# Optimization experiments

Hardware: AMD Instinct MI355X
Metric: run time of the kernel (lower is better)

Reference implementation:

```python
import jax, jax.numpy as jnp
import numpy as np

EMBED_DIM = 1024
NUM_HEADS = 16
HEAD_DIM = EMBED_DIM // NUM_HEADS


def setup_inputs() -> dict:
    key = jax.random.key(0)
    ks = jax.random.split(key, 10)
    B, S, E = 2, 2048, EMBED_DIM
    scale = 1.0 / np.sqrt(E)
    x = jax.random.normal(ks[0], (B, S, E), dtype=jnp.float32)
    mask = jax.random.randint(ks[1], (B, 1, S, S), 0, 2, dtype=jnp.int32)
    # Linear weights stored as [in, out] (transposed torch layout for x @ W)
    Wq = jax.random.normal(ks[2], (E, E), dtype=jnp.float32) * scale
    bq = jnp.zeros((E,), dtype=jnp.float32)
    Wk = jax.random.normal(ks[3], (E, E), dtype=jnp.float32) * scale
    bk = jnp.zeros((E,), dtype=jnp.float32)
    Wv = jax.random.normal(ks[4], (E, E), dtype=jnp.float32) * scale
    bv = jnp.zeros((E,), dtype=jnp.float32)
    Wo = jax.random.normal(ks[5], (E, E), dtype=jnp.float32) * scale
    bo = jnp.zeros((E,), dtype=jnp.float32)
    return {"x": x, "mask": mask, "Wq": Wq, "bq": bq, "Wk": Wk, "bk": bk,
            "Wv": Wv, "bv": bv, "Wo": Wo, "bo": bo}


def _heads(t, B, S):
    # [B, S, E] -> [B, H, S, Dh]
    return t.reshape(B, S, NUM_HEADS, HEAD_DIM).transpose(0, 2, 1, 3)


def reference(x, mask, Wq, bq, Wk, bk, Wv, bv, Wo, bo):
    B, S, E = x.shape
    q = _heads(x @ Wq + bq, B, S)
    k = _heads(x @ Wk + bk, B, S)
    v = _heads(x @ Wv + bv, B, S)
    inv_sqrt_dk = 1.0 / jnp.sqrt(jnp.asarray(HEAD_DIM, dtype=x.dtype))
    # scores: [B, H, S, S]
    scores = jnp.einsum('bhqd,bhkd->bhqk', q, k) * inv_sqrt_dk
    scores = jnp.where(mask == 0, jnp.asarray(-1e9, dtype=scores.dtype), scores)
    p = jax.nn.softmax(scores, axis=-1)
    ctx = jnp.einsum('bhqk,bhkd->bhqd', p, v)  # [B, H, S, Dh]
    ctx = ctx.transpose(0, 2, 1, 3).reshape(B, S, E)
    return ctx @ Wo + bo
```

## Files before the change

### kernel.cpp

```cpp
#include <hip/hip_runtime.h>

typedef float f32x4 __attribute__((ext_vector_type(4)));
typedef short s16x8 __attribute__((ext_vector_type(8)));
typedef unsigned short u16;
typedef unsigned short u16x4 __attribute__((ext_vector_type(4)));
typedef unsigned int u32x2 __attribute__((ext_vector_type(2)));

#define DI __device__ __forceinline__

constexpr int B_ = 2, S_ = 2048, E_ = 1024, H_ = 16, DH = 64, M_ = B_ * S_;
constexpr float QSCALE = 0.125f * 1.4426950408889634f;

DI u16 f2bf(float f) {
    unsigned u = __float_as_uint(f);
    u += 0x7fffu + ((u >> 16) & 1u);
    return (u16)(u >> 16);
}

DI unsigned cvtpk(float lo, float hi) {
    unsigned r;
    asm("v_cvt_pk_bf16_f32 %0, %1, %2" : "=v"(r) : "v"(lo), "v"(hi));
    return r;
}

DI void mfma(f32x4& d, s16x8 a, s16x8 b) {
    asm("v_mfma_f32_16x16x32_bf16 %0, %1, %2, %0" : "+v"(d) : "v"(a), "v"(b));
}

typedef __attribute__((address_space(1))) const void gas_cv;
typedef __attribute__((address_space(3))) void las_v;
DI void gl16(const void* g, void* l) {
    __builtin_amdgcn_global_load_lds((gas_cv*)g, (las_v*)l, 16, 0, 0);
}


__global__ __launch_bounds__(256) void cvt_bf16(const float* __restrict__ in,
                                                u16* __restrict__ out, int n4) {
    int i = blockIdx.x * 256 + threadIdx.x;
    if (i < n4) {
        float4 v = ((const float4*)in)[i];
        u16x4 o;
        o.x = f2bf(v.x); o.y = f2bf(v.y); o.z = f2bf(v.z); o.w = f2bf(v.w);
        ((u16x4*)out)[i] = o;
    }
}

__global__ __launch_bounds__(256) void wtrans(const float* __restrict__ in,
                                              u16* __restrict__ out) {
    __shared__ float t[64][65];
    int k0 = blockIdx.x * 64, n0 = blockIdx.y * 64;
    int tx = threadIdx.x & 63, ty = threadIdx.x >> 6;
#pragma unroll
    for (int i = 0; i < 16; i++) {
        int r = i * 4 + ty;
        t[r][tx] = in[(k0 + r) * E_ + n0 + tx];
    }
    __syncthreads();
#pragma unroll
    for (int i = 0; i < 16; i++) {
        int r = i * 4 + ty;
        out[(n0 + r) * E_ + k0 + tx] = f2bf(t[tx][r]);
    }
}

__global__ __launch_bounds__(256) void mpackK(const int* __restrict__ mask,
                                              unsigned* __restrict__ mk) {
    int t = blockIdx.x * 256 + threadIdx.x;
    int q = t & (S_ - 1);
    int kw = (t >> 11) & 63;
    int b = t >> 17;
    const int* mp = mask + ((size_t)(b * S_ + q)) * S_ + kw * 32;
    unsigned w = 0;
#pragma unroll
    for (int j = 0; j < 32; j++) w |= (mp[j] != 0 ? 1u : 0u) << j;
    mk[t] = w;
}

template <int MODE>
__global__ __launch_bounds__(256) void proj(const u16* __restrict__ A,
                                            const u16* __restrict__ Bt,
                                            const float* __restrict__ b0,
                                            const float* __restrict__ b1,
                                            const float* __restrict__ b2,
                                            u16* __restrict__ Qh, u16* __restrict__ Kh,
                                            u16* __restrict__ Vt,
                                            float* __restrict__ of) {
    __shared__ u16 sA[128 * 32], sB[128 * 32];
    const int tid = threadIdx.x, lane = tid & 63, wid = tid >> 6;
    const int g = lane >> 4, lr = lane & 15;
    const int wr = wid >> 1, wc = wid & 1;
    constexpr int NCT = (MODE == 0) ? 24 : 8;
    const int nblk = (M_ / 128) * NCT;
    const int cpx = nblk / 8;
    const int sw = (blockIdx.x & 7) * cpx + (blockIdx.x >> 3);
    const int rt = sw / NCT, ct = sw % NCT;
    const int row0 = rt * 128, col0 = ct * 128;

    const int srow = wid * 32 + (lane >> 2);
    const int scol = (lane & 3) * 8;

    f32x4 acc[4][4] = {};
    for (int kt = 0; kt < E_ / 32; kt++) {
        int k0 = kt * 32;
        __syncthreads();
#pragma unroll
        for (int j = 0; j < 2; j++) {
            gl16(A  + (size_t)(row0 + srow + j * 16) * E_ + k0 + scol,
                 sA + wid * 1024 + j * 512);
            gl16(Bt + (size_t)(col0 + srow + j * 16) * E_ + k0 + scol,
                 sB + wid * 1024 + j * 512);
        }
        __syncthreads();
        s16x8 af[4], bfr[4];
#pragma unroll
        for (int m = 0; m < 4; m++)
            af[m] = *(const s16x8*)(sA + (wr * 64 + m * 16 + lr) * 32 + g * 8);
#pragma unroll
        for (int n = 0; n < 4; n++)
            bfr[n] = *(const s16x8*)(sB + (wc * 64 + n * 16 + lr) * 32 + g * 8);
        __builtin_amdgcn_s_setprio(1);
#pragma unroll
        for (int m = 0; m < 4; m++)
#pragma unroll
            for (int n = 0; n < 4; n++) mfma(acc[m][n], af[m], bfr[n]);
        __builtin_amdgcn_s_setprio(0);
    }

    if constexpr (MODE == 3) {
#pragma unroll
        for (int n = 0; n < 4; n++) {
            int c = col0 + wc * 64 + n * 16 + lr;
            float bb = b0[c];
#pragma unroll
            for (int m = 0; m < 4; m++) {
                int rb = row0 + wr * 64 + m * 16 + g * 4;
#pragma unroll
                for (int i = 0; i < 4; i++) of[(size_t)(rb + i) * E_ + c] = acc[m][n][i] + bb;
            }
        }
    } else {
        const int region = col0 >> 10;
        const float* bias = region == 0 ? b0 : (region == 1 ? b1 : b2);
        const float scl = region == 0 ? QSCALE : 1.0f;
        u16* dst = region == 0 ? Qh : Kh;
#pragma unroll
        for (int n = 0; n < 4; n++) {
            int ccol = (col0 & 1023) + wc * 64 + n * 16 + lr;
            float bb = bias[ccol];
            int h = ccol >> 6, dh = ccol & 63;
#pragma unroll
            for (int m = 0; m < 4; m++) {
                int rb = row0 + wr * 64 + m * 16 + g * 4;
                int b = rb >> 11, s = rb & (S_ - 1);
                if (region == 2) {
                    u16x4 pk;
                    pk.x = f2bf(acc[m][n][0] + bb);
                    pk.y = f2bf(acc[m][n][1] + bb);
                    pk.z = f2bf(acc[m][n][2] + bb);
                    pk.w = f2bf(acc[m][n][3] + bb);
                    *(u16x4*)(Vt + ((size_t)((b * H_ + h) * DH + dh)) * S_ + s) = pk;
                } else {
#pragma unroll
                    for (int i = 0; i < 4; i++) {
                        int r = rb + i, bb2 = r >> 11, s2 = r & (S_ - 1);
                        dst[((size_t)((bb2 * H_ + h) * S_) + s2) * DH + dh] =
                            f2bf((acc[m][n][i] + bb) * scl);
                    }
                }
            }
        }
    }
}

__global__ __launch_bounds__(256, 4) void attn(const u16* __restrict__ Q,
                                               const u16* __restrict__ K,
                                               const u16* __restrict__ V,
                                               const unsigned* __restrict__ mk,
                                               u16* __restrict__ ctx) {
    __shared__ u16 sK[2][64 * 64];
    __shared__ u16 sV[2][64 * 64];
    __shared__ u16 sP[4][16 * 64];
    const int tid = threadIdx.x, lane = tid & 63, wid = tid >> 6;
    const int g = lane >> 4, lr = lane & 15, swz = lr & 7;
    const int swg = (blockIdx.x & 7) * 128 + (blockIdx.x >> 3);
    const int q0 = (swg & 31) * 64, h = (swg >> 5) & 15, b = swg >> 9;
    const u16* qb = Q + ((size_t)(b * H_ + h) * S_ + q0) * DH;
    const u16* kb = K + (size_t)(b * H_ + h) * S_ * DH;
    const u16* vb = V + (size_t)(b * H_ + h) * DH * S_;
    const unsigned* mkb = mk + (size_t)b * (S_ / 32) * S_;
    const int qrow = q0 + wid * 16 + lr;
    u16* sPw = sP[wid];

    s16x8 qf[2];
#pragma unroll
    for (int dc = 0; dc < 2; dc++)
        qf[dc] = *(const s16x8*)(qb + (wid * 16 + lr) * DH + dc * 32 + g * 8);

    f32x4 o[4] = {};
    float mrun = -3e38f, lrun = 0.f;
    s16x8 kv[2], vv[2];

#pragma unroll
    for (int p = 0; p < 2; p++) {
        int L = p * 256 + tid;
        kv[p] = *(const s16x8*)(kb + (L >> 3) * DH + (L & 7) * 8);
        vv[p] = *(const s16x8*)(vb + (L >> 3) * S_ + (L & 7) * 8);
    }
#pragma unroll
    for (int p = 0; p < 2; p++) {
        int L = p * 256 + tid;
        int rr = L >> 3, cc = L & 7;
        *(s16x8*)(sK[0] + rr * 64 + (cc ^ (rr & 7)) * 8) = kv[p];
        *(s16x8*)(sV[0] + rr * 64 + (cc ^ (rr & 7)) * 8) = vv[p];
    }
    __syncthreads();

    int cur = 0;
    for (int kt = 0; kt < S_ / 64; kt++) {
        const int k0 = kt * 64;
        if (kt < S_ / 64 - 1) {
            const int kn = k0 + 64;
#pragma unroll
            for (int p = 0; p < 2; p++) {
                int L = p * 256 + tid;
                kv[p] = *(const s16x8*)(kb + (kn + (L >> 3)) * DH + (L & 7) * 8);
                vv[p] = *(const s16x8*)(vb + (L >> 3) * S_ + kn + (L & 7) * 8);
            }
        }
        unsigned mw[2];
#pragma unroll
        for (int nw = 0; nw < 2; nw++)
            mw[nw] = mkb[((k0 >> 5) + nw) * S_ + qrow];

        const u16* sKc = sK[cur];
        const u16* sVc = sV[cur];
        f32x4 sc[4];
        __builtin_amdgcn_s_setprio(1);
#pragma unroll
        for (int n = 0; n < 4; n++) {
            const u16* kr = sKc + (n * 16 + lr) * 64;
            s16x8 kf0 = *(const s16x8*)(kr + (g ^ swz) * 8);
            s16x8 kf1 = *(const s16x8*)(kr + ((4 + g) ^ swz) * 8);
            f32x4 z = {0.f, 0.f, 0.f, 0.f};
            sc[n] = z;
            mfma(sc[n], kf0, qf[0]);
            mfma(sc[n], kf1, qf[1]);
        }
        __builtin_amdgcn_s_setprio(0);

#pragma unroll
        for (int n = 0; n < 4; n++) {
            unsigned sb = mw[n >> 1] >> ((n & 1) * 16 + g * 4);
#pragma unroll
            for (int i = 0; i < 4; i++)
                if (!((sb >> i) & 1u)) sc[n][i] = -1e9f;
        }
        float vm = -3e38f;
#pragma unroll
        for (int n = 0; n < 4; n++)
#pragma unroll
            for (int i = 0; i < 4; i++) vm = fmaxf(vm, sc[n][i]);
        vm = fmaxf(vm, __shfl_xor(vm, 16));
        vm = fmaxf(vm, __shfl_xor(vm, 32));
        if (!__all(vm <= mrun + 8.f)) {
            float mnew = fmaxf(mrun, vm);
            float fac = exp2f(mrun - mnew);
            mrun = mnew;
#pragma unroll
            for (int n = 0; n < 4; n++) o[n] *= fac;
            lrun *= fac;
        }
        float rs = 0.f;
#pragma unroll
        for (int n = 0; n < 4; n++)
#pragma unroll
            for (int i = 0; i < 4; i++) {
                float pv = exp2f(sc[n][i] - mrun);
                sc[n][i] = pv;
                rs += pv;
            }
        rs += __shfl_xor(rs, 16);
        rs += __shfl_xor(rs, 32);
        lrun += rs;
#pragma unroll
        for (int n = 0; n < 4; n++) {
            u32x2 wp;
            wp.x = cvtpk(sc[n][0], sc[n][1]);
            wp.y = cvtpk(sc[n][2], sc[n][3]);
            int unit = (n * 2 + (g >> 1)) ^ swz;
            *(u32x2*)(sPw + lr * 64 + unit * 8 + (g & 1) * 4) = wp;
        }
        __builtin_amdgcn_s_setprio(1);
#pragma unroll
        for (int kc = 0; kc < 2; kc++) {
            s16x8 pb = *(const s16x8*)(sPw + lr * 64 + ((kc * 4 + g) ^ swz) * 8);
#pragma unroll
            for (int n = 0; n < 4; n++) {
                int rv = n * 16 + lr;
                s16x8 vf = *(const s16x8*)(sVc + rv * 64 + ((kc * 4 + g) ^ (rv & 7)) * 8);
                mfma(o[n], vf, pb);
            }
        }
        __builtin_amdgcn_s_setprio(0);
        if (kt < S_ / 64 - 1) {
#pragma unroll
            for (int p = 0; p < 2; p++) {
                int L = p * 256 + tid;
                int rr = L >> 3, cc = L & 7;
                *(s16x8*)(sK[cur ^ 1] + rr * 64 + (cc ^ (rr & 7)) * 8) = kv[p];
                *(s16x8*)(sV[cur ^ 1] + rr * 64 + (cc ^ (rr & 7)) * 8) = vv[p];
            }
            __syncthreads();
            cur ^= 1;
        }
    }
    {
        float inv = 1.f / lrun;
#pragma unroll
        for (int n = 0; n < 4; n++) {
            u16x4 pk;
#pragma unroll
            for (int i = 0; i < 4; i++) pk[i] = f2bf(o[n][i] * inv);
            *(u16x4*)(sPw + lr * 64 + n * 16 + g * 4) = pk;
        }
#pragma unroll
        for (int half = 0; half < 2; half++) {
            int rr = half * 8 + (lane >> 3);
            s16x8 v = *(const s16x8*)(sPw + rr * 64 + (lane & 7) * 8);
            int q = q0 + wid * 16 + rr;
            *(s16x8*)(ctx + ((size_t)(b * S_ + q)) * E_ + h * DH + (lane & 7) * 8) = v;
        }
    }
}


extern "C" void kernel_launch(void* const* d_in, const int* in_sizes, int n_in,
                              void* d_out, int out_size, void* d_ws, size_t ws_size,
                              hipStream_t stream) {
    const float* x  = (const float*)d_in[0];
    const int* mask = (const int*)d_in[1];
    const float* Wq = (const float*)d_in[2]; const float* bq = (const float*)d_in[3];
    const float* Wk = (const float*)d_in[4]; const float* bk = (const float*)d_in[5];
    const float* Wv = (const float*)d_in[6]; const float* bv = (const float*)d_in[7];
    const float* Wo = (const float*)d_in[8]; const float* bo = (const float*)d_in[9];
    float* out = (float*)d_out;

    char* ws = (char*)d_ws;
    u16* xb     = (u16*)(ws);
    u16* Wqkvt  = (u16*)(ws + (8u  << 20));
    u16* Wot    = (u16*)(ws + (14u << 20));
    u16* Qh     = (u16*)(ws + (16u << 20));
    u16* Kh     = (u16*)(ws + (24u << 20));
    u16* Vt     = (u16*)(ws + (32u << 20));
    u16* ctx    = (u16*)(ws + (40u << 20));
    unsigned* mk = (unsigned*)(ws + (48u << 20));

    cvt_bf16<<<(M_ * E_ / 4 + 255) / 256, 256, 0, stream>>>(x, xb, M_ * E_ / 4);
    dim3 tg(E_ / 64, E_ / 64);
    wtrans<<<tg, 256, 0, stream>>>(Wq, Wqkvt);
    wtrans<<<tg, 256, 0, stream>>>(Wk, Wqkvt + 1024 * 1024);
    wtrans<<<tg, 256, 0, stream>>>(Wv, Wqkvt + 2 * 1024 * 1024);
    wtrans<<<tg, 256, 0, stream>>>(Wo, Wot);
    mpackK<<<(B_ * 64 * S_) / 256, 256, 0, stream>>>(mask, mk);

    proj<0><<<(M_ / 128) * (3072 / 128), 256, 0, stream>>>(xb, Wqkvt, bq, bk, bv,
                                                           Qh, Kh, Vt, nullptr);

    attn<<<(S_ / 64) * H_ * B_, 256, 0, stream>>>(Qh, Kh, Vt, mk, ctx);

    proj<3><<<(M_ / 128) * (E_ / 128), 256, 0, stream>>>(ctx, Wot, bo, nullptr, nullptr,
                                                         nullptr, nullptr, nullptr, out);
}
```

Measured before the change: 166.5 us.

## Apply mask via bf16 AND masks, MFMA row sums, and K=64 GEMM tiles

```diff
diff --git a/kernel.cpp b/kernel.cpp
--- a/kernel.cpp
+++ b/kernel.cpp
@@ -20,6 +20,12 @@
 DI unsigned cvtpk(float lo, float hi) {
     unsigned r;
     asm("v_cvt_pk_bf16_f32 %0, %1, %2" : "=v"(r) : "v"(lo), "v"(hi));
+    return r;
+}
+
+DI float max3f(float a, float b, float c) {
+    float r;
+    asm("v_max3_f32 %0, %1, %2, %3" : "=v"(r) : "v"(a), "v"(b), "v"(c));
     return r;
 }
 
@@ -63,17 +69,11 @@
     }
 }
 
-__global__ __launch_bounds__(256) void mpackK(const int* __restrict__ mask,
-                                              unsigned* __restrict__ mk) {
-    int t = blockIdx.x * 256 + threadIdx.x;
-    int q = t & (S_ - 1);
-    int kw = (t >> 11) & 63;
-    int b = t >> 17;
-    const int* mp = mask + ((size_t)(b * S_ + q)) * S_ + kw * 32;
-    unsigned w = 0;
-#pragma unroll
-    for (int j = 0; j < 32; j++) w |= (mp[j] != 0 ? 1u : 0u) << j;
-    mk[t] = w;
+__global__ __launch_bounds__(256) void mexpand(const int* __restrict__ mask,
+                                               unsigned* __restrict__ mexp) {
+    int i = blockIdx.x * 256 + threadIdx.x;
+    int2 mv = ((const int2*)mask)[i];
+    mexp[i] = (mv.x ? 0xFFFFu : 0u) | (mv.y ? 0xFFFF0000u : 0u);
 }
 
 template <int MODE>
@@ -85,7 +85,7 @@
                                             u16* __restrict__ Qh, u16* __restrict__ Kh,
                                             u16* __restrict__ Vt,
                                             float* __restrict__ of) {
-    __shared__ u16 sA[128 * 32], sB[128 * 32];
+    __shared__ u16 sA[128 * 64], sB[128 * 64];
     const int tid = threadIdx.x, lane = tid & 63, wid = tid >> 6;
     const int g = lane >> 4, lr = lane & 15;
     const int wr = wid >> 1, wc = wid & 1;
@@ -96,34 +96,36 @@
     const int rt = sw / NCT, ct = sw % NCT;
     const int row0 = rt * 128, col0 = ct * 128;
 
-    const int srow = wid * 32 + (lane >> 2);
-    const int scol = (lane & 3) * 8;
+    const int srow = lane >> 3;
+    const int scol = (lane & 7) * 8;
 
     f32x4 acc[4][4] = {};
-    for (int kt = 0; kt < E_ / 32; kt++) {
-        int k0 = kt * 32;
+    for (int kt = 0; kt < E_ / 64; kt++) {
+        int k0 = kt * 64;
         __syncthreads();
 #pragma unroll
-        for (int j = 0; j < 2; j++) {
-            gl16(A  + (size_t)(row0 + srow + j * 16) * E_ + k0 + scol,
-                 sA + wid * 1024 + j * 512);
-            gl16(Bt + (size_t)(col0 + srow + j * 16) * E_ + k0 + scol,
-                 sB + wid * 1024 + j * 512);
+        for (int j = 0; j < 4; j++) {
+            int r = wid * 32 + j * 8;
+            gl16(A  + (size_t)(row0 + r + srow) * E_ + k0 + scol, sA + r * 64);
+            gl16(Bt + (size_t)(col0 + r + srow) * E_ + k0 + scol, sB + r * 64);
         }
         __syncthreads();
-        s16x8 af[4], bfr[4];
-#pragma unroll
-        for (int m = 0; m < 4; m++)
-            af[m] = *(const s16x8*)(sA + (wr * 64 + m * 16 + lr) * 32 + g * 8);
-#pragma unroll
-        for (int n = 0; n < 4; n++)
-            bfr[n] = *(const s16x8*)(sB + (wc * 64 + n * 16 + lr) * 32 + g * 8);
-        __builtin_amdgcn_s_setprio(1);
-#pragma unroll
-        for (int m = 0; m < 4; m++)
-#pragma unroll
-            for (int n = 0; n < 4; n++) mfma(acc[m][n], af[m], bfr[n]);
-        __builtin_amdgcn_s_setprio(0);
+#pragma unroll
+        for (int kk = 0; kk < 2; kk++) {
+            s16x8 af[4], bfr[4];
+#pragma unroll
+            for (int m = 0; m < 4; m++)
+                af[m] = *(const s16x8*)(sA + (wr * 64 + m * 16 + lr) * 64 + kk * 32 + g * 8);
+#pragma unroll
+            for (int n = 0; n < 4; n++)
+                bfr[n] = *(const s16x8*)(sB + (wc * 64 + n * 16 + lr) * 64 + kk * 32 + g * 8);
+            __builtin_amdgcn_s_setprio(1);
+#pragma unroll
+            for (int m = 0; m < 4; m++)
+#pragma unroll
+                for (int n = 0; n < 4; n++) mfma(acc[m][n], af[m], bfr[n]);
+            __builtin_amdgcn_s_setprio(0);
+        }
     }
 
     if constexpr (MODE == 3) {
@@ -175,7 +177,7 @@
 __global__ __launch_bounds__(256, 4) void attn(const u16* __restrict__ Q,
                                                const u16* __restrict__ K,
                                                const u16* __restrict__ V,
-                                               const unsigned* __restrict__ mk,
+                                               const unsigned* __restrict__ mexp,
                                                u16* __restrict__ ctx) {
     __shared__ u16 sK[2][64 * 64];
     __shared__ u16 sV[2][64 * 64];
@@ -187,8 +189,8 @@
     const u16* qb = Q + ((size_t)(b * H_ + h) * S_ + q0) * DH;
     const u16* kb = K + (size_t)(b * H_ + h) * S_ * DH;
     const u16* vb = V + (size_t)(b * H_ + h) * DH * S_;
-    const unsigned* mkb = mk + (size_t)b * (S_ / 32) * S_;
     const int qrow = q0 + wid * 16 + lr;
+    const unsigned* mq = mexp + (size_t)(b * S_ + qrow) * (S_ / 2);
     u16* sPw = sP[wid];
 
     s16x8 qf[2];
@@ -196,8 +198,14 @@
     for (int dc = 0; dc < 2; dc++)
         qf[dc] = *(const s16x8*)(qb + (wid * 16 + lr) * DH + dc * 32 + g * 8);
 
+    const u16 ov = (lr == 0) ? (u16)0x3F80 : (u16)0;
+    s16x8 ones;
+#pragma unroll
+    for (int i = 0; i < 8; i++) ones[i] = (short)ov;
+
     f32x4 o[4] = {};
-    float mrun = -3e38f, lrun = 0.f;
+    f32x4 ol = {};
+    float mrun = -3e38f;
     s16x8 kv[2], vv[2];
 
 #pragma unroll
@@ -227,10 +235,10 @@
                 vv[p] = *(const s16x8*)(vb + (L >> 3) * S_ + kn + (L & 7) * 8);
             }
         }
-        unsigned mw[2];
-#pragma unroll
-        for (int nw = 0; nw < 2; nw++)
-            mw[nw] = mkb[((k0 >> 5) + nw) * S_ + qrow];
+        u32x2 mm[4];
+#pragma unroll
+        for (int n = 0; n < 4; n++)
+            mm[n] = *(const u32x2*)(mq + (k0 >> 1) + n * 8 + g * 2);
 
         const u16* sKc = sK[cur];
         const u16* sVc = sV[cur];
@@ -248,45 +256,28 @@
         }
         __builtin_amdgcn_s_setprio(0);
 
-#pragma unroll
-        for (int n = 0; n < 4; n++) {
-            unsigned sb = mw[n >> 1] >> ((n & 1) * 16 + g * 4);
-#pragma unroll
-            for (int i = 0; i < 4; i++)
-                if (!((sb >> i) & 1u)) sc[n][i] = -1e9f;
-        }
-        float vm = -3e38f;
-#pragma unroll
-        for (int n = 0; n < 4; n++)
-#pragma unroll
-            for (int i = 0; i < 4; i++) vm = fmaxf(vm, sc[n][i]);
+        float t0 = max3f(sc[0][0], sc[0][1], sc[0][2]);
+        float t1 = max3f(sc[0][3], sc[1][0], sc[1][1]);
+        float t2 = max3f(sc[1][2], sc[1][3], sc[2][0]);
+        float t3 = max3f(sc[2][1], sc[2][2], sc[2][3]);
+        float t4 = max3f(sc[3][0], sc[3][1], sc[3][2]);
+        float vm = fmaxf(max3f(max3f(t0, t1, sc[3][3]), t3, t4), t2);
         vm = fmaxf(vm, __shfl_xor(vm, 16));
         vm = fmaxf(vm, __shfl_xor(vm, 32));
         if (!__all(vm <= mrun + 8.f)) {
-            float mnew = fmaxf(mrun, vm);
-            float fac = exp2f(mrun - mnew);
-            mrun = mnew;
+            float fac = __builtin_amdgcn_exp2f(mrun - vm);
+            mrun = fmaxf(mrun, vm);
 #pragma unroll
             for (int n = 0; n < 4; n++) o[n] *= fac;
-            lrun *= fac;
-        }
-        float rs = 0.f;
-#pragma unroll
-        for (int n = 0; n < 4; n++)
-#pragma unroll
-            for (int i = 0; i < 4; i++) {
-                float pv = exp2f(sc[n][i] - mrun);
-                sc[n][i] = pv;
-                rs += pv;
-            }
-        rs += __shfl_xor(rs, 16);
-        rs += __shfl_xor(rs, 32);
-        lrun += rs;
+            ol *= fac;
+        }
 #pragma unroll
         for (int n = 0; n < 4; n++) {
             u32x2 wp;
-            wp.x = cvtpk(sc[n][0], sc[n][1]);
-            wp.y = cvtpk(sc[n][2], sc[n][3]);
+            wp.x = cvtpk(__builtin_amdgcn_exp2f(sc[n][0] - mrun),
+                         __builtin_amdgcn_exp2f(sc[n][1] - mrun)) & mm[n].x;
+            wp.y = cvtpk(__builtin_amdgcn_exp2f(sc[n][2] - mrun),
+                         __builtin_amdgcn_exp2f(sc[n][3] - mrun)) & mm[n].y;
             int unit = (n * 2 + (g >> 1)) ^ swz;
             *(u32x2*)(sPw + lr * 64 + unit * 8 + (g & 1) * 4) = wp;
         }
@@ -294,6 +285,7 @@
 #pragma unroll
         for (int kc = 0; kc < 2; kc++) {
             s16x8 pb = *(const s16x8*)(sPw + lr * 64 + ((kc * 4 + g) ^ swz) * 8);
+            mfma(ol, ones, pb);
 #pragma unroll
             for (int n = 0; n < 4; n++) {
                 int rv = n * 16 + lr;
@@ -315,7 +307,8 @@
         }
     }
     {
-        float inv = 1.f / lrun;
+        float lsum = __shfl(ol[0], lr);
+        float inv = 1.f / lsum;
 #pragma unroll
         for (int n = 0; n < 4; n++) {
             u16x4 pk;
@@ -353,7 +346,7 @@
     u16* Kh     = (u16*)(ws + (24u << 20));
     u16* Vt     = (u16*)(ws + (32u << 20));
     u16* ctx    = (u16*)(ws + (40u << 20));
-    unsigned* mk = (unsigned*)(ws + (48u << 20));
+    unsigned* mexp = (unsigned*)(ws + (48u << 20));
 
     cvt_bf16<<<(M_ * E_ / 4 + 255) / 256, 256, 0, stream>>>(x, xb, M_ * E_ / 4);
     dim3 tg(E_ / 64, E_ / 64);
@@ -361,12 +354,12 @@
     wtrans<<<tg, 256, 0, stream>>>(Wk, Wqkvt + 1024 * 1024);
     wtrans<<<tg, 256, 0, stream>>>(Wv, Wqkvt + 2 * 1024 * 1024);
     wtrans<<<tg, 256, 0, stream>>>(Wo, Wot);
-    mpackK<<<(B_ * 64 * S_) / 256, 256, 0, stream>>>(mask, mk);
+    mexpand<<<(B_ * S_ * S_ / 2) / 256, 256, 0, stream>>>(mask, mexp);
 
     proj<0><<<(M_ / 128) * (3072 / 128), 256, 0, stream>>>(xb, Wqkvt, bq, bk, bv,
                                                            Qh, Kh, Vt, nullptr);
 
-    attn<<<(S_ / 64) * H_ * B_, 256, 0, stream>>>(Qh, Kh, Vt, mk, ctx);
+    attn<<<(S_ / 64) * H_ * B_, 256, 0, stream>>>(Qh, Kh, Vt, mexp, ctx);
 
     proj<3><<<(M_ / 128) * (E_ / 128), 256, 0, stream>>>(ctx, Wot, bo, nullptr, nullptr,
                                                          nullptr, nullptr, nullptr, out);
```

Result: slower. 176.0 us (+5.7%).
